# Kernel tuning notes

Measured on AMD Instinct MI355X. Metric: run time of the kernel, lower is better.

## Reference

```python
import jax, jax.numpy as jnp
import numpy as np

N_NODES = 100000
N_EDGES = 1600000
IN_DIM, HID_DIM, OUT_DIM = 128, 128, 64


def setup_inputs() -> dict:
    key = jax.random.key(0)
    ks = jax.random.split(key, 5)
    x = jax.random.normal(ks[0], (N_NODES, IN_DIM), dtype=jnp.float32)
    edge_index = jax.random.randint(ks[1], (2, N_EDGES), 0, N_NODES, dtype=jnp.int64)
    W1 = jax.random.normal(ks[2], (IN_DIM, HID_DIM), dtype=jnp.float32) * (1.0 / np.sqrt(IN_DIM))
    b1 = jnp.zeros((HID_DIM,), dtype=jnp.float32)
    W2 = jax.random.normal(ks[3], (HID_DIM, OUT_DIM), dtype=jnp.float32) * (1.0 / np.sqrt(HID_DIM))
    b2 = jnp.zeros((OUT_DIM,), dtype=jnp.float32)
    return {"x": x, "edge_index": edge_index, "W1": W1, "b1": b1, "W2": W2, "b2": b2}


def _gcn_conv(h, row, col, norm, b, n_nodes):
    # h: [N, F] already linearly transformed; message = norm_e * h[src]; scatter-add to dst
    msg = h[row] * norm[:, None]                      # [E+N, F]
    out = jax.ops.segment_sum(msg, col, num_segments=n_nodes)
    return out + b


def reference(x, edge_index, W1, b1, W2, b2):
    n = x.shape[0]
    loops = jnp.arange(n, dtype=edge_index.dtype)
    row = jnp.concatenate([edge_index[0], loops])     # sources (incl. self loops)
    col = jnp.concatenate([edge_index[1], loops])     # targets
    # symmetric normalization: deg over targets with unit edge weights
    deg = jax.ops.segment_sum(jnp.ones_like(col, dtype=x.dtype), col, num_segments=n)
    dinv = jnp.where(deg > 0, jax.lax.rsqrt(jnp.maximum(deg, 1.0)), 0.0)
    norm = dinv[row] * dinv[col]                      # [E+N]
    h = jax.nn.relu(_gcn_conv(x @ W1, row, col, norm, b1, n))
    out = _gcn_conv(h @ W2, row, col, norm, b2, n)
    return out.mean(axis=0)                           # [OUT_DIM]
```

## Files before the change

kernel.cpp:

```cpp
#include <hip/hip_runtime.h>

#define N_NODES 100000
#define N_EDGES 1600000
#define IN_DIM 128
#define HID_DIM 128
#define OUT_DIM 64
#define BKT_SHIFT 8
#define BKT_SIZE 256
#define NBKT ((N_NODES + BKT_SIZE - 1) / BKT_SIZE)
#define B1 256
#define HIST_N (NBKT * B1)
#define HIST_N2 (2 * HIST_N)

typedef float v2f __attribute__((ext_vector_type(2)));

__device__ __forceinline__ void load4(const void* ei, int is64, int half, int base,
                                      int* v) {
  if (is64) {
    const long long* e = (const long long*)ei + (size_t)half * N_EDGES + base;
    longlong2 a = *(const longlong2*)e;
    longlong2 b = *(const longlong2*)(e + 2);
    v[0] = (int)a.x; v[1] = (int)a.y; v[2] = (int)b.x; v[3] = (int)b.y;
  } else {
    const int* e = (const int*)ei + (size_t)half * N_EDGES + base;
    int4 a = *(const int4*)e;
    v[0] = a.x; v[1] = a.y; v[2] = a.z; v[3] = a.w;
  }
}

__global__ void detect_kernel(const unsigned int* ei, int* flag, float* S) {
  __shared__ int nz;
  if (threadIdx.x == 0) nz = 0;
  __syncthreads();
  unsigned int v = ei[1 + 2 * threadIdx.x];
  if (v != 0u) nz = 1;
  if (threadIdx.x < HID_DIM) S[threadIdx.x] = 0.f;
  __syncthreads();
  if (threadIdx.x == 0) *flag = (nz == 0) ? 1 : 0;
}

__global__ __launch_bounds__(256) void hist_kernel(const void* ei, const int* flag,
                                                   int* hist) {
  __shared__ int hd[NBKT], hs[NBKT];
  for (int k = threadIdx.x; k < NBKT; k += 256) { hd[k] = 0; hs[k] = 0; }
  __syncthreads();
  const int is64 = *flag;
  for (int g = blockIdx.x * 256 + threadIdx.x; g < N_EDGES / 4; g += B1 * 256) {
    int r[4], c[4];
    load4(ei, is64, 0, g * 4, r);
    load4(ei, is64, 1, g * 4, c);
#pragma unroll
    for (int k = 0; k < 4; k++) {
      atomicAdd(&hd[c[k] >> BKT_SHIFT], 1);
      atomicAdd(&hs[r[k] >> BKT_SHIFT], 1);
    }
  }
  __syncthreads();
  for (int k = threadIdx.x; k < NBKT; k += 256) {
    hist[k * B1 + blockIdx.x] = hd[k];
    hist[HIST_N + k * B1 + blockIdx.x] = hs[k];
  }
}

__global__ void scan1_kernel(const int* cnt, int* part, int* bsum, int n) {
  __shared__ int tmp[256];
  int i = blockIdx.x * 256 + threadIdx.x;
  int v = (i < n) ? cnt[i] : 0;
  tmp[threadIdx.x] = v;
  __syncthreads();
  for (int off = 1; off < 256; off <<= 1) {
    int t2 = (threadIdx.x >= off) ? tmp[threadIdx.x - off] : 0;
    __syncthreads();
    tmp[threadIdx.x] += t2;
    __syncthreads();
  }
  if (i < n) part[i] = tmp[threadIdx.x] - v;
  if (threadIdx.x == 255) bsum[blockIdx.x] = tmp[255];
}

__global__ void scan2_kernel(int* bsum, int nb) {
  __shared__ int tmp[1024];
  int v = (threadIdx.x < nb) ? bsum[threadIdx.x] : 0;
  tmp[threadIdx.x] = v;
  __syncthreads();
  for (int off = 1; off < 1024; off <<= 1) {
    int t2 = (threadIdx.x >= off) ? tmp[threadIdx.x - off] : 0;
    __syncthreads();
    tmp[threadIdx.x] += t2;
    __syncthreads();
  }
  if (threadIdx.x < nb) bsum[threadIdx.x] = tmp[threadIdx.x] - v;
}

__global__ void scan3_kernel(int* arr, const int* bsum, int n) {
  int i = blockIdx.x * 256 + threadIdx.x;
  if (i < n) arr[i] += bsum[blockIdx.x];
}

__global__ __launch_bounds__(256) void scatter_kernel(const void* ei, const int* flag,
                                                      const int* hist,
                                                      unsigned int* pairs) {
  __shared__ int cd[NBKT], cs[NBKT];
  for (int k = threadIdx.x; k < NBKT; k += 256) {
    cd[k] = hist[k * B1 + blockIdx.x];
    cs[k] = hist[HIST_N + k * B1 + blockIdx.x];
  }
  __syncthreads();
  const int is64 = *flag;
  for (int g = blockIdx.x * 256 + threadIdx.x; g < N_EDGES / 4; g += B1 * 256) {
    int r[4], c[4];
    load4(ei, is64, 0, g * 4, r);
    load4(ei, is64, 1, g * 4, c);
#pragma unroll
    for (int k = 0; k < 4; k++) {
      int pd = atomicAdd(&cd[c[k] >> BKT_SHIFT], 1);
      pairs[pd] = ((unsigned int)(c[k] & (BKT_SIZE - 1)) << 17) | (unsigned int)r[k];
      int ps = atomicAdd(&cs[r[k] >> BKT_SHIFT], 1);
      pairs[ps] = ((unsigned int)(r[k] & (BKT_SIZE - 1)) << 17) | (unsigned int)c[k];
    }
  }
}

__global__ __launch_bounds__(256) void csr_kernel(const int* hist,
                                                  const unsigned int* pairs,
                                                  int* rowptr, int* csr, float* dinv) {
  __shared__ int cnt[BKT_SIZE], sc[BKT_SIZE], cur[BKT_SIZE];
  const int k = blockIdx.x;
  const int base = hist[k * B1];
  const int end = (k == NBKT - 1) ? N_EDGES : hist[(k + 1) * B1];
  const int nseg = end - base;
  const int l = threadIdx.x;
  cnt[l] = 0;
  __syncthreads();
  for (int i = l; i < nseg; i += 256) atomicAdd(&cnt[pairs[base + i] >> 17], 1);
  __syncthreads();
  sc[l] = cnt[l];
  __syncthreads();
  for (int off = 1; off < BKT_SIZE; off <<= 1) {
    int v = (l >= off) ? sc[l - off] : 0;
    __syncthreads();
    sc[l] += v;
    __syncthreads();
  }
  {
    int excl = sc[l] - cnt[l];
    cur[l] = base + excl;
    int v = k * BKT_SIZE + l;
    if (v < N_NODES) {
      rowptr[v] = base + excl;
      dinv[v] = rsqrtf((float)(cnt[l] + 1));
    }
  }
  if (k == NBKT - 1 && l == 0) rowptr[N_NODES] = N_EDGES;
  __syncthreads();
  for (int i = l; i < nseg; i += 256) {
    unsigned int pk = pairs[base + i];
    int pos = atomicAdd(&cur[pk >> 17], 1);
    csr[pos] = (int)(pk & 0x1FFFFu);
  }
}

__global__ __launch_bounds__(256) void outsum_kernel(const int* hist,
                                                     const unsigned int* pairs,
                                                     const float* __restrict__ dinv,
                                                     float* wacc) {
  __shared__ float fb[BKT_SIZE];
  const int k = blockIdx.x;
  const int base = hist[HIST_N + k * B1];
  const int end = (k == NBKT - 1) ? 2 * N_EDGES : hist[HIST_N + (k + 1) * B1];
  fb[threadIdx.x] = 0.f;
  __syncthreads();
  for (int i = base + threadIdx.x; i < end; i += 256) {
    unsigned int pk = pairs[i];
    atomicAdd(&fb[pk >> 17], dinv[pk & 0x1FFFFu]);
  }
  __syncthreads();
  int v = k * BKT_SIZE + threadIdx.x;
  if (v < N_NODES) wacc[v] = fb[threadIdx.x];
}

__global__ __launch_bounds__(256) void gemm_kernel(const float* __restrict__ x,
                                                   const float* __restrict__ W,
                                                   const float* __restrict__ dinv,
                                                   unsigned int* __restrict__ G) {
  __shared__ float lx[64 * IN_DIM];
  __shared__ float lw[32 * HID_DIM];
  const int t = threadIdx.x;
  const int row0 = blockIdx.x * 64;
  const int nrow = min(64, N_NODES - row0);

  {
    const float4* x4 = (const float4*)(x + (size_t)row0 * IN_DIM);
    float4* lx4 = (float4*)lx;
    const int tot = nrow * (IN_DIM / 4);
    for (int i = t; i < tot; i += 256) lx4[i] = x4[i];
  }

  const int c0 = (t & 31) * 4;
  const int rbase = (t >> 5) * 8;
  float4 acc[8];
#pragma unroll
  for (int i = 0; i < 8; i++) acc[i] = make_float4(0.f, 0.f, 0.f, 0.f);

  for (int kc = 0; kc < IN_DIM; kc += 32) {
    __syncthreads();
    {
      const float4* W4 = (const float4*)(W + (size_t)kc * HID_DIM);
      float4* lw4 = (float4*)lw;
      for (int i = t; i < 32 * HID_DIM / 4; i += 256) lw4[i] = W4[i];
    }
    __syncthreads();
#pragma unroll
    for (int kk = 0; kk < 32; kk += 4) {
      float4 xv[8];
#pragma unroll
      for (int i = 0; i < 8; i++)
        xv[i] = *(const float4*)&lx[(rbase + i) * IN_DIM + kc + kk];
#pragma unroll
      for (int j = 0; j < 4; j++) {
        float4 wv = *(const float4*)&lw[(kk + j) * HID_DIM + c0];
#pragma unroll
        for (int i = 0; i < 8; i++) {
          float xs = (j == 0) ? xv[i].x : (j == 1) ? xv[i].y : (j == 2) ? xv[i].z : xv[i].w;
          acc[i].x += xs * wv.x;
          acc[i].y += xs * wv.y;
          acc[i].z += xs * wv.z;
          acc[i].w += xs * wv.w;
        }
      }
    }
  }
#pragma unroll
  for (int i = 0; i < 8; i++) {
    int r = row0 + rbase + i;
    if (r < N_NODES) {
      float d = dinv[r];
      float4 v = acc[i];
      int pk = __builtin_amdgcn_cvt_pk_fp8_f32(v.x * d, v.y * d, 0, false);
      pk = __builtin_amdgcn_cvt_pk_fp8_f32(v.z * d, v.w * d, pk, true);
      G[(size_t)r * (HID_DIM / 4) + (c0 >> 2)] = (unsigned int)pk;
    }
  }
}

__global__ __launch_bounds__(256) void aggregate_kernel(
    const unsigned int* __restrict__ G, const int* __restrict__ rowptr,
    const int* __restrict__ csr, const float* __restrict__ dinv,
    const float* __restrict__ wacc, const float* __restrict__ b1,
    float* __restrict__ S) {
  const int lane = threadIdx.x & 63;
  const int sub = lane & 31;
  const int half = lane >> 5;
  const int wid = blockIdx.x * (blockDim.x >> 6) + (threadIdx.x >> 6);
  const int nwaves = gridDim.x * (blockDim.x >> 6);
  const float4 b = ((const float4*)b1)[sub];
  v2f sacc01 = {0.f, 0.f}, sacc23 = {0.f, 0.f};

  for (int c = wid; c < N_NODES; c += nwaves) {
    const int start = rowptr[c];
    const int cnum = rowptr[c + 1] - start;
    v2f a01 = {0.f, 0.f}, a23 = {0.f, 0.f};
    if (half == 0) {
      unsigned int g = G[c * 32 + sub];
      a01 = __builtin_amdgcn_cvt_pk_f32_fp8((int)g, false);
      a23 = __builtin_amdgcn_cvt_pk_f32_fp8((int)g, true);
    }
    for (int j0 = 0; j0 < cnum; j0 += 64) {
      int src = 0;
      if (j0 + lane < cnum) src = csr[start + j0 + lane];
      const int m = min(64, cnum - j0);
      int i = 0;
      for (; i + 8 <= m; i += 8) {
        int s0 = __shfl(src, i + half);
        int s1 = __shfl(src, i + 2 + half);
        int s2 = __shfl(src, i + 4 + half);
        int s3 = __shfl(src, i + 6 + half);
        unsigned int g0 = G[s0 * 32 + sub];
        unsigned int g1 = G[s1 * 32 + sub];
        unsigned int g2 = G[s2 * 32 + sub];
        unsigned int g3 = G[s3 * 32 + sub];
        a01 += __builtin_amdgcn_cvt_pk_f32_fp8((int)g0, false) +
               __builtin_amdgcn_cvt_pk_f32_fp8((int)g1, false);
        a23 += __builtin_amdgcn_cvt_pk_f32_fp8((int)g0, true) +
               __builtin_amdgcn_cvt_pk_f32_fp8((int)g1, true);
        a01 += __builtin_amdgcn_cvt_pk_f32_fp8((int)g2, false) +
               __builtin_amdgcn_cvt_pk_f32_fp8((int)g3, false);
        a23 += __builtin_amdgcn_cvt_pk_f32_fp8((int)g2, true) +
               __builtin_amdgcn_cvt_pk_f32_fp8((int)g3, true);
      }
      for (; i + 2 <= m; i += 2) {
        int s = __shfl(src, i + half);
        unsigned int g = G[s * 32 + sub];
        a01 += __builtin_amdgcn_cvt_pk_f32_fp8((int)g, false);
        a23 += __builtin_amdgcn_cvt_pk_f32_fp8((int)g, true);
      }
      if (i < m) {
        int s = __shfl(src, i);
        if (half == 0) {
          unsigned int g = G[s * 32 + sub];
          a01 += __builtin_amdgcn_cvt_pk_f32_fp8((int)g, false);
          a23 += __builtin_amdgcn_cvt_pk_f32_fp8((int)g, true);
        }
      }
    }
    a01.x += __shfl(a01.x, sub + 32);
    a01.y += __shfl(a01.y, sub + 32);
    a23.x += __shfl(a23.x, sub + 32);
    a23.y += __shfl(a23.y, sub + 32);
    if (half == 0) {
      float d = dinv[c];
      float wc = d * (wacc[c] + d);
      sacc01.x += wc * fmaxf(fmaf(d, a01.x, b.x), 0.f);
      sacc01.y += wc * fmaxf(fmaf(d, a01.y, b.y), 0.f);
      sacc23.x += wc * fmaxf(fmaf(d, a23.x, b.z), 0.f);
      sacc23.y += wc * fmaxf(fmaf(d, a23.y, b.w), 0.f);
    }
  }

  __shared__ float ls[HID_DIM];
  if (threadIdx.x < HID_DIM) ls[threadIdx.x] = 0.f;
  __syncthreads();
  if (half == 0) {
    atomicAdd(&ls[4 * sub + 0], sacc01.x);
    atomicAdd(&ls[4 * sub + 1], sacc01.y);
    atomicAdd(&ls[4 * sub + 2], sacc23.x);
    atomicAdd(&ls[4 * sub + 3], sacc23.y);
  }
  __syncthreads();
  if (threadIdx.x < HID_DIM) atomicAdd(&S[threadIdx.x], ls[threadIdx.x]);
}

__global__ void finish_kernel(const float* __restrict__ S, const float* __restrict__ W2,
                              const float* __restrict__ b2, float* __restrict__ out) {
  int j = threadIdx.x;
  float acc = 0.f;
  for (int k = 0; k < HID_DIM; k++) acc += S[k] * W2[k * OUT_DIM + j];
  out[j] = acc * (1.0f / N_NODES) + b2[j];
}

extern "C" void kernel_launch(void* const* d_in, const int* in_sizes, int n_in,
                              void* d_out, int out_size, void* d_ws, size_t ws_size,
                              hipStream_t stream) {
  const float* x  = (const float*)d_in[0];
  const void*  ei = d_in[1];
  const float* W1 = (const float*)d_in[2];
  const float* b1 = (const float*)d_in[3];
  const float* W2 = (const float*)d_in[4];
  const float* b2 = (const float*)d_in[5];
  float* out = (float*)d_out;

  char* p = (char*)d_ws;
  size_t off = 0;
  auto alloc = [&](size_t bytes) -> void* {
    void* r = p + off;
    off = (off + bytes + 63) & ~(size_t)63;
    return r;
  };
  int*   flag   = (int*)alloc(64);
  int*   hist   = (int*)alloc((size_t)HIST_N2 * 4);
  int*   bsum   = (int*)alloc(1024 * 4);
  unsigned int* pairs = (unsigned int*)alloc((size_t)2 * N_EDGES * 4);
  int*   rowptr = (int*)alloc(((size_t)N_NODES + 1) * 4);
  int*   csr    = (int*)alloc((size_t)N_EDGES * 4);
  float* dinv   = (float*)alloc((size_t)N_NODES * 4);
  float* wacc   = (float*)alloc((size_t)N_NODES * 4);
  float* S      = (float*)alloc(HID_DIM * 4);
  unsigned int* G = (unsigned int*)alloc((size_t)N_NODES * HID_DIM);
  (void)ws_size; (void)n_in; (void)in_sizes; (void)out_size;

  const int NBH = HIST_N2 / 256;

  detect_kernel<<<1, 256, 0, stream>>>((const unsigned int*)ei, flag, S);
  hist_kernel<<<B1, 256, 0, stream>>>(ei, flag, hist);
  scan1_kernel<<<NBH, 256, 0, stream>>>(hist, hist, bsum, HIST_N2);
  scan2_kernel<<<1, 1024, 0, stream>>>(bsum, NBH);
  scan3_kernel<<<NBH, 256, 0, stream>>>(hist, bsum, HIST_N2);
  scatter_kernel<<<B1, 256, 0, stream>>>(ei, flag, hist, pairs);
  csr_kernel<<<NBKT, 256, 0, stream>>>(hist, pairs, rowptr, csr, dinv);
  outsum_kernel<<<NBKT, 256, 0, stream>>>(hist, pairs, dinv, wacc);
  gemm_kernel<<<(N_NODES + 63) / 64, 256, 0, stream>>>(x, W1, dinv, G);
  aggregate_kernel<<<2048, 256, 0, stream>>>(G, rowptr, csr, dinv, wacc, b1, S);
  finish_kernel<<<1, 64, 0, stream>>>(S, W2, b2, out);
}
```

Measured before the change: 299.1 us.

## Use bf16 MFMA for first GEMM and slice feature columns in aggregation

The fp32 scalar GEMM is replaced by a bf16 MFMA 16x16x32 kernel that converts x and a transposed W1 to bf16 in shared memory, using 128-row tiles and writing fp8 results byte by byte. The aggregation kernel now splits the 128 feature columns into four slices across blocks, so each wave gathers a 32-byte slice per neighbour, with 8 lanes per edge and 8 edges in flight. It also reduces with xor shuffles and loads CSR indices non-temporally. The intent is to cut GEMM compute time and improve gather locality and cache reuse, at the cost of bf16 input rounding, byte-granular stores, and four passes over the CSR per node.

```diff
diff --git a/kernel.cpp b/kernel.cpp
--- a/kernel.cpp
+++ b/kernel.cpp
@@ -13,6 +13,13 @@
 #define HIST_N2 (2 * HIST_N)
 
 typedef float v2f __attribute__((ext_vector_type(2)));
+typedef float v4f __attribute__((ext_vector_type(4)));
+typedef short v8s __attribute__((ext_vector_type(8)));
+
+__device__ __forceinline__ unsigned int f2bf(float f) {
+  unsigned int u = __float_as_uint(f);
+  return (u + 0x7FFFu + ((u >> 16) & 1u)) >> 16;
+}
 
 __device__ __forceinline__ void load4(const void* ei, int is64, int half, int base,
                                       int* v) {
@@ -183,64 +190,85 @@
                                                    const float* __restrict__ W,
                                                    const float* __restrict__ dinv,
                                                    unsigned int* __restrict__ G) {
-  __shared__ float lx[64 * IN_DIM];
-  __shared__ float lw[32 * HID_DIM];
+  __shared__ __align__(16) unsigned short lx[128][136];
+  __shared__ __align__(16) unsigned short lwt[128][136];
   const int t = threadIdx.x;
-  const int row0 = blockIdx.x * 64;
-  const int nrow = min(64, N_NODES - row0);
-
+  const int row0 = blockIdx.x * 128;
+
+  {
+    const float4* W4 = (const float4*)W;
+    for (int it = 0; it < 16; ++it) {
+      int idx = t + 256 * it;
+      int k = idx >> 5, c4 = (idx & 31) * 4;
+      float4 w = W4[idx];
+      lwt[c4 + 0][k] = (unsigned short)f2bf(w.x);
+      lwt[c4 + 1][k] = (unsigned short)f2bf(w.y);
+      lwt[c4 + 2][k] = (unsigned short)f2bf(w.z);
+      lwt[c4 + 3][k] = (unsigned short)f2bf(w.w);
+    }
+  }
   {
     const float4* x4 = (const float4*)(x + (size_t)row0 * IN_DIM);
-    float4* lx4 = (float4*)lx;
-    const int tot = nrow * (IN_DIM / 4);
-    for (int i = t; i < tot; i += 256) lx4[i] = x4[i];
-  }
-
-  const int c0 = (t & 31) * 4;
-  const int rbase = (t >> 5) * 8;
-  float4 acc[8];
-#pragma unroll
-  for (int i = 0; i < 8; i++) acc[i] = make_float4(0.f, 0.f, 0.f, 0.f);
-
-  for (int kc = 0; kc < IN_DIM; kc += 32) {
-    __syncthreads();
-    {
-      const float4* W4 = (const float4*)(W + (size_t)kc * HID_DIM);
-      float4* lw4 = (float4*)lw;
-      for (int i = t; i < 32 * HID_DIM / 4; i += 256) lw4[i] = W4[i];
-    }
-    __syncthreads();
-#pragma unroll
-    for (int kk = 0; kk < 32; kk += 4) {
-      float4 xv[8];
-#pragma unroll
-      for (int i = 0; i < 8; i++)
-        xv[i] = *(const float4*)&lx[(rbase + i) * IN_DIM + kc + kk];
-#pragma unroll
-      for (int j = 0; j < 4; j++) {
-        float4 wv = *(const float4*)&lw[(kk + j) * HID_DIM + c0];
-#pragma unroll
-        for (int i = 0; i < 8; i++) {
-          float xs = (j == 0) ? xv[i].x : (j == 1) ? xv[i].y : (j == 2) ? xv[i].z : xv[i].w;
-          acc[i].x += xs * wv.x;
-          acc[i].y += xs * wv.y;
-          acc[i].z += xs * wv.z;
-          acc[i].w += xs * wv.w;
+    for (int it = 0; it < 16; ++it) {
+      int idx = t + 256 * it;
+      int r = idx >> 5, kq = (idx & 31) * 4;
+      float4 v = make_float4(0.f, 0.f, 0.f, 0.f);
+      if (row0 + r < N_NODES) v = x4[idx];
+      unsigned int p0 = (f2bf(v.y) << 16) | f2bf(v.x);
+      unsigned int p1 = (f2bf(v.w) << 16) | f2bf(v.z);
+      *(uint2*)&lx[r][kq] = make_uint2(p0, p1);
+    }
+  }
+  __syncthreads();
+
+  const int lane = t & 63;
+  const int wv = t >> 6;
+  const int m0 = wv * 32;
+  const int lrow = lane & 15;
+  const int lk = (lane >> 4) * 8;
+
+  v4f acc[2][8];
+#pragma unroll
+  for (int si = 0; si < 2; si++)
+#pragma unroll
+    for (int n = 0; n < 8; n++) acc[si][n] = (v4f){0.f, 0.f, 0.f, 0.f};
+
+#pragma unroll
+  for (int kk = 0; kk < 128; kk += 32) {
+    v8s a0 = *(const v8s*)&lx[m0 + lrow][kk + lk];
+    v8s a1 = *(const v8s*)&lx[m0 + 16 + lrow][kk + lk];
+#pragma unroll
+    for (int n = 0; n < 8; n++) {
+      v8s b = *(const v8s*)&lwt[n * 16 + lrow][kk + lk];
+      acc[0][n] = __builtin_amdgcn_mfma_f32_16x16x32_bf16(a0, b, acc[0][n], 0, 0, 0);
+      acc[1][n] = __builtin_amdgcn_mfma_f32_16x16x32_bf16(a1, b, acc[1][n], 0, 0, 0);
+    }
+  }
+
+  unsigned char* G8 = (unsigned char*)G;
+  float dv[2][4];
+#pragma unroll
+  for (int si = 0; si < 2; si++)
+#pragma unroll
+    for (int i = 0; i < 4; i++) {
+      int r = row0 + m0 + si * 16 + (lane >> 4) * 4 + i;
+      dv[si][i] = (r < N_NODES) ? dinv[r] : 0.f;
+    }
+#pragma unroll
+  for (int si = 0; si < 2; si++)
+#pragma unroll
+    for (int n = 0; n < 8; n++) {
+      int colg = n * 16 + (lane & 15);
+#pragma unroll
+      for (int i = 0; i < 4; i++) {
+        int r = row0 + m0 + si * 16 + (lane >> 4) * 4 + i;
+        if (r < N_NODES) {
+          float v = acc[si][n][i] * dv[si][i];
+          int pk = __builtin_amdgcn_cvt_pk_fp8_f32(v, v, 0, false);
+          G8[(size_t)r * HID_DIM + colg] = (unsigned char)(pk & 0xFF);
         }
       }
     }
-  }
-#pragma unroll
-  for (int i = 0; i < 8; i++) {
-    int r = row0 + rbase + i;
-    if (r < N_NODES) {
-      float d = dinv[r];
-      float4 v = acc[i];
-      int pk = __builtin_amdgcn_cvt_pk_fp8_f32(v.x * d, v.y * d, 0, false);
-      pk = __builtin_amdgcn_cvt_pk_fp8_f32(v.z * d, v.w * d, pk, true);
-      G[(size_t)r * (HID_DIM / 4) + (c0 >> 2)] = (unsigned int)pk;
-    }
-  }
 }
 
 __global__ __launch_bounds__(256) void aggregate_kernel(
@@ -249,85 +277,78 @@
     const float* __restrict__ wacc, const float* __restrict__ b1,
     float* __restrict__ S) {
   const int lane = threadIdx.x & 63;
-  const int sub = lane & 31;
-  const int half = lane >> 5;
-  const int wid = blockIdx.x * (blockDim.x >> 6) + (threadIdx.x >> 6);
-  const int nwaves = gridDim.x * (blockDim.x >> 6);
-  const float4 b = ((const float4*)b1)[sub];
-  v2f sacc01 = {0.f, 0.f}, sacc23 = {0.f, 0.f};
-
-  for (int c = wid; c < N_NODES; c += nwaves) {
+  const int grp = lane >> 3;
+  const int dwo = lane & 7;
+  const int slice = blockIdx.x & 3;
+  const int sbase = slice * 8;
+  const int wid = (blockIdx.x >> 2) * 4 + (threadIdx.x >> 6);
+  const int nw = (gridDim.x >> 2) * 4;
+  const float4 b = ((const float4*)b1)[sbase + dwo];
+  v2f s01 = {0.f, 0.f}, s23 = {0.f, 0.f};
+
+  for (int c = wid; c < N_NODES; c += nw) {
     const int start = rowptr[c];
     const int cnum = rowptr[c + 1] - start;
     v2f a01 = {0.f, 0.f}, a23 = {0.f, 0.f};
-    if (half == 0) {
-      unsigned int g = G[c * 32 + sub];
+    if (grp == 0) {
+      unsigned int g = G[c * 32 + sbase + dwo];
       a01 = __builtin_amdgcn_cvt_pk_f32_fp8((int)g, false);
       a23 = __builtin_amdgcn_cvt_pk_f32_fp8((int)g, true);
     }
     for (int j0 = 0; j0 < cnum; j0 += 64) {
       int src = 0;
-      if (j0 + lane < cnum) src = csr[start + j0 + lane];
+      if (j0 + lane < cnum)
+        src = __builtin_nontemporal_load(&csr[start + j0 + lane]);
       const int m = min(64, cnum - j0);
       int i = 0;
-      for (; i + 8 <= m; i += 8) {
-        int s0 = __shfl(src, i + half);
-        int s1 = __shfl(src, i + 2 + half);
-        int s2 = __shfl(src, i + 4 + half);
-        int s3 = __shfl(src, i + 6 + half);
-        unsigned int g0 = G[s0 * 32 + sub];
-        unsigned int g1 = G[s1 * 32 + sub];
-        unsigned int g2 = G[s2 * 32 + sub];
-        unsigned int g3 = G[s3 * 32 + sub];
+      for (; i + 16 <= m; i += 16) {
+        int s0 = __shfl(src, i + grp);
+        int s1 = __shfl(src, i + 8 + grp);
+        unsigned int g0 = G[s0 * 32 + sbase + dwo];
+        unsigned int g1 = G[s1 * 32 + sbase + dwo];
         a01 += __builtin_amdgcn_cvt_pk_f32_fp8((int)g0, false) +
                __builtin_amdgcn_cvt_pk_f32_fp8((int)g1, false);
         a23 += __builtin_amdgcn_cvt_pk_f32_fp8((int)g0, true) +
                __builtin_amdgcn_cvt_pk_f32_fp8((int)g1, true);
-        a01 += __builtin_amdgcn_cvt_pk_f32_fp8((int)g2, false) +
-               __builtin_amdgcn_cvt_pk_f32_fp8((int)g3, false);
-        a23 += __builtin_amdgcn_cvt_pk_f32_fp8((int)g2, true) +
-               __builtin_amdgcn_cvt_pk_f32_fp8((int)g3, true);
       }
-      for (; i + 2 <= m; i += 2) {
-        int s = __shfl(src, i + half);
-        unsigned int g = G[s * 32 + sub];
-        a01 += __builtin_amdgcn_cvt_pk_f32_fp8((int)g, false);
-        a23 += __builtin_amdgcn_cvt_pk_f32_fp8((int)g, true);
-      }
-      if (i < m) {
-        int s = __shfl(src, i);
-        if (half == 0) {
-          unsigned int g = G[s * 32 + sub];
+      for (; i < m; i += 8) {
+        int e = i + grp;
+        int s = __shfl(src, min(e, m - 1));
+        if (e < m) {
+          unsigned int g = G[s * 32 + sbase + dwo];
           a01 += __builtin_amdgcn_cvt_pk_f32_fp8((int)g, false);
           a23 += __builtin_amdgcn_cvt_pk_f32_fp8((int)g, true);
         }
       }
     }
-    a01.x += __shfl(a01.x, sub + 32);
-    a01.y += __shfl(a01.y, sub + 32);
-    a23.x += __shfl(a23.x, sub + 32);
-    a23.y += __shfl(a23.y, sub + 32);
-    if (half == 0) {
+#pragma unroll
+    for (int off = 8; off < 64; off <<= 1) {
+      a01.x += __shfl_xor(a01.x, off);
+      a01.y += __shfl_xor(a01.y, off);
+      a23.x += __shfl_xor(a23.x, off);
+      a23.y += __shfl_xor(a23.y, off);
+    }
+    if (grp == 0) {
       float d = dinv[c];
       float wc = d * (wacc[c] + d);
-      sacc01.x += wc * fmaxf(fmaf(d, a01.x, b.x), 0.f);
-      sacc01.y += wc * fmaxf(fmaf(d, a01.y, b.y), 0.f);
-      sacc23.x += wc * fmaxf(fmaf(d, a23.x, b.z), 0.f);
-      sacc23.y += wc * fmaxf(fmaf(d, a23.y, b.w), 0.f);
-    }
-  }
-
-  __shared__ float ls[HID_DIM];
-  if (threadIdx.x < HID_DIM) ls[threadIdx.x] = 0.f;
-  __syncthreads();
-  if (half == 0) {
-    atomicAdd(&ls[4 * sub + 0], sacc01.x);
-    atomicAdd(&ls[4 * sub + 1], sacc01.y);
-    atomicAdd(&ls[4 * sub + 2], sacc23.x);
-    atomicAdd(&ls[4 * sub + 3], sacc23.y);
-  }
-  __syncthreads();
-  if (threadIdx.x < HID_DIM) atomicAdd(&S[threadIdx.x], ls[threadIdx.x]);
+      s01.x += wc * fmaxf(fmaf(d, a01.x, b.x), 0.f);
+      s01.y += wc * fmaxf(fmaf(d, a01.y, b.y), 0.f);
+      s23.x += wc * fmaxf(fmaf(d, a23.x, b.z), 0.f);
+      s23.y += wc * fmaxf(fmaf(d, a23.y, b.w), 0.f);
+    }
+  }
+
+  __shared__ float ls[32];
+  if (threadIdx.x < 32) ls[threadIdx.x] = 0.f;
+  __syncthreads();
+  if (grp == 0) {
+    atomicAdd(&ls[dwo * 4 + 0], s01.x);
+    atomicAdd(&ls[dwo * 4 + 1], s01.y);
+    atomicAdd(&ls[dwo * 4 + 2], s23.x);
+    atomicAdd(&ls[dwo * 4 + 3], s23.y);
+  }
+  __syncthreads();
+  if (threadIdx.x < 32) atomicAdd(&S[slice * 32 + threadIdx.x], ls[threadIdx.x]);
 }
 
 __global__ void finish_kernel(const float* __restrict__ S, const float* __restrict__ W2,
@@ -378,7 +399,7 @@
   scatter_kernel<<<B1, 256, 0, stream>>>(ei, flag, hist, pairs);
   csr_kernel<<<NBKT, 256, 0, stream>>>(hist, pairs, rowptr, csr, dinv);
   outsum_kernel<<<NBKT, 256, 0, stream>>>(hist, pairs, dinv, wacc);
-  gemm_kernel<<<(N_NODES + 63) / 64, 256, 0, stream>>>(x, W1, dinv, G);
+  gemm_kernel<<<(N_NODES + 127) / 128, 256, 0, stream>>>(x, W1, dinv, G);
   aggregate_kernel<<<2048, 256, 0, stream>>>(G, rowptr, csr, dinv, wacc, b1, S);
   finish_kernel<<<1, 64, 0, stream>>>(S, W2, b2, out);
 }
```

After: 333.3 us. 11.4% more time.
